# Performance work log

Measured on AMD Instinct MI355X. Metric: run time of the kernel, lower is better.

## Reference

```python
import jax, jax.numpy as jnp
import numpy as np

B = 512          # batch
SD = 1           # series_dim
FEAT = 8         # features_dim
IN = SD + FEAT   # inputs_dim
R = 32           # residual_channels (= skip_channels)
NB, NL = 3, 8
NLAYERS = NB * NL  # 24
L = 256          # cached queue length (>= max dilation 128)
HID = 128        # hidden_size


def setup_inputs() -> dict:
    key = jax.random.key(0)
    ks = jax.random.split(key, 13)
    s = 0.1
    return {
        "x": jax.random.normal(ks[0], (B, SD, 1), jnp.float32),
        "features": jax.random.normal(ks[1], (B, FEAT, 1), jnp.float32),
        "queues": jax.random.normal(ks[2], (NLAYERS, B, R, L), jnp.float32),
        "fc_h_w": jax.random.normal(ks[3], (R, IN), jnp.float32) * s,
        "fc_h_b": jax.random.normal(ks[4], (R,), jnp.float32) * s,
        "fc_c_w": jax.random.normal(ks[5], (R, IN), jnp.float32) * s,
        "fc_c_b": jax.random.normal(ks[6], (R,), jnp.float32) * s,
        "conv_w": jax.random.normal(ks[7], (NLAYERS, 4 * R, R, 2), jnp.float32) * s,
        "conv_b": jax.random.normal(ks[8], (NLAYERS, 4 * R), jnp.float32) * s,
        "fc1_w": jax.random.normal(ks[9], (HID, NLAYERS * R), jnp.float32) * s,
        "fc1_b": jax.random.normal(ks[10], (HID,), jnp.float32) * s,
        "fc2_w": jax.random.normal(ks[11], (SD, HID), jnp.float32) * s,
        "fc2_b": jax.random.normal(ks[12], (SD,), jnp.float32) * s,
    }


def reference(x, features, queues, fc_h_w, fc_h_b, fc_c_w, fc_c_b,
              conv_w, conv_b, fc1_w, fc1_b, fc2_w, fc2_b):
    # inputs: cat over channels at the single decode timestep -> [B, IN]
    inp = jnp.concatenate([x, features], axis=1)[:, :, 0]
    h0 = jnp.tanh(inp @ fc_h_w.T + fc_h_b)   # [B, R]
    c0 = jnp.tanh(inp @ fc_c_w.T + fc_c_b)   # [B, R]

    # dilations 2^0..2^7 repeated for each block; gather the cached sample
    # state[:, :, L-1-(dilation-1)] == state[:, :, L-dilation] for each layer
    dils = jnp.array([2 ** d for _ in range(NB) for d in range(NL)], jnp.int32)
    past = queues[jnp.arange(NLAYERS), :, :, L - dils]   # [NLAYERS, B, R]

    def step(carry, layer):
        h, c = carry
        W, b, p = layer                 # W:[4R,R,2], b:[4R], p:[B,R]
        # kernel-size-2 causal conv on the two timesteps (past, current)
        out = p @ W[:, :, 0].T + h @ W[:, :, 1].T + b    # [B, 4R]
        ig, cf, cg, eg = jnp.split(out, 4, axis=1)
        c = jax.nn.sigmoid(ig) * c + jnp.tanh(cf) * jax.nn.sigmoid(cg)
        h = jax.nn.sigmoid(eg) * jnp.tanh(c)
        return (h, c), h

    (_, _), skips = jax.lax.scan(step, (h0, c0), (conv_w, conv_b, past))
    # skips: [NLAYERS, B, R] -> torch cat(dim=1) order -> [B, NLAYERS*R]
    skips_flat = jnp.transpose(skips, (1, 0, 2)).reshape(B, NLAYERS * R)

    y_hidden = jax.nn.relu(skips_flat @ fc1_w.T + fc1_b)
    h_hat = (y_hidden @ fc2_w.T + fc2_b)[:, :, None]     # [B, SD, 1]

    # update_queues: layer i appends the h ENTERING layer i (h0, then skips[:-1])
    h_seq = jnp.concatenate([h0[None], skips[:-1]], axis=0)  # [NLAYERS, B, R]
    update_queues = jnp.concatenate([queues, h_seq[:, :, :, None]], axis=3)
    return h_hat, update_queues
```

## Files before the change

kernel.cpp:

```cpp
#include <hip/hip_runtime.h>
#include <math.h>

#define B 512
#define FEAT 8
#define IN 9
#define R 32
#define NLAYERS 24
#define L 256
#define HID 128

#define SCAN_BLOCKS 128
#define COPY_BLOCKS 2048
#define ROWS (NLAYERS * B * R)
#define OUTQ_FLOATS (ROWS * 257)
#define NQ (OUTQ_FLOATS / 4)

__device__ __forceinline__ float sigmoidf_(float x) {
    return 1.0f / (1.0f + __expf(-x));
}
__device__ __forceinline__ float tanhf_(float x) {
    float a = __expf(2.0f * fabsf(x));
    float r = 1.0f - 2.0f / (a + 1.0f);
    return copysignf(r, x);
}

__global__ __launch_bounds__(256) void wavedec_scan(
    const float* __restrict__ x, const float* __restrict__ features,
    const float* __restrict__ queues,
    const float* __restrict__ fc_h_w, const float* __restrict__ fc_h_b,
    const float* __restrict__ fc_c_w, const float* __restrict__ fc_c_b,
    const float* __restrict__ conv_w, const float* __restrict__ conv_b,
    const float* __restrict__ fc1_w, const float* __restrict__ fc1_b,
    const float* __restrict__ fc2_w, const float* __restrict__ fc2_b,
    float* __restrict__ out)
{
    const int tid  = threadIdx.x;
    const int lane = tid & 63;
    const int wid  = tid >> 6;
    float* outq = out + B;

    const int b = blockIdx.x * 4 + wid;
    const int r = lane & 31;
    __shared__ __align__(16) float sk[4][NLAYERS * R];

    float inp[IN];
    inp[0] = x[b];
    #pragma unroll
    for (int i = 0; i < FEAT; i++) inp[1 + i] = features[b * FEAT + i];
    float ah = fc_h_b[r], ac = fc_c_b[r];
    #pragma unroll
    for (int i = 0; i < IN; i++) {
        ah += inp[i] * fc_h_w[r * IN + i];
        ac += inp[i] * fc_c_w[r * IN + i];
    }
    float h = tanhf_(ah);
    float c = tanhf_(ac);

    for (int l = 0; l < NLAYERS; l++) {
        const int dil = 1 << (l & 7);
        const int base = (l * B + b) * R;

        if (lane < 32) outq[(long)(base + r) * 257 + 256] = h;

        float p = queues[(long)(base + r) * 256 + (256 - dil)];

        const float* W0 = conv_w + ((long)l * 128 + lane) * 64;
        const float* W1 = W0 + 64 * 64;
        float acc0 = conv_b[l * 128 + lane];
        float acc1 = conv_b[l * 128 + lane + 64];
        #pragma unroll
        for (int rr = 0; rr < 32; rr += 2) {
            float4 wa = *(const float4*)(W0 + rr * 2);
            float4 wb = *(const float4*)(W1 + rr * 2);
            float h0v = __shfl(h, rr),     p0v = __shfl(p, rr);
            float h1v = __shfl(h, rr + 1), p1v = __shfl(p, rr + 1);
            acc0 += p0v * wa.x + h0v * wa.y + p1v * wa.z + h1v * wa.w;
            acc1 += p0v * wb.x + h0v * wb.y + p1v * wb.z + h1v * wb.w;
        }
        float cf = __shfl(acc0, r + 32);
        float eg = __shfl(acc1, r + 32);
        c = sigmoidf_(acc0) * c + tanhf_(cf) * sigmoidf_(acc1);
        h = sigmoidf_(eg) * tanhf_(c);

        if (lane < 32) sk[wid][l * R + r] = h;
    }
    __syncthreads();

    const float* w1a = fc1_w + (long)lane * 768;
    const float* w1b = fc1_w + (long)(lane + 64) * 768;
    const float* skp = sk[wid];
    float ya = fc1_b[lane], yb = fc1_b[lane + 64];
    for (int i = 0; i < 768; i += 4) {
        float4 s  = *(const float4*)(skp + i);
        float4 a4 = *(const float4*)(w1a + i);
        float4 b4 = *(const float4*)(w1b + i);
        ya += s.x * a4.x + s.y * a4.y + s.z * a4.z + s.w * a4.w;
        yb += s.x * b4.x + s.y * b4.y + s.z * b4.z + s.w * b4.w;
    }
    ya = fmaxf(ya, 0.0f);
    yb = fmaxf(yb, 0.0f);
    float v = ya * fc2_w[lane] + yb * fc2_w[lane + 64];
    #pragma unroll
    for (int off = 32; off; off >>= 1) v += __shfl_xor(v, off);
    if (lane == 0) out[b] = v + fc2_b[0];
}

__global__ __launch_bounds__(256) void wavedec_copy(
    const float* __restrict__ queues, float* __restrict__ out)
{
    float* __restrict__ outq = out + B;
    const uint32_t stride = gridDim.x * blockDim.x;
    for (uint32_t q = blockIdx.x * blockDim.x + threadIdx.x; q < (uint32_t)NQ; q += stride) {
        const uint32_t o   = q << 2;
        const uint32_t row = (uint32_t)(((uint64_t)o * 4278255361ull) >> 40);
        const uint32_t col = o - row * 257u;
        float v[4];
        #pragma unroll
        for (int i = 0; i < 4; i++) {
            uint32_t r2 = row, c2 = col + (uint32_t)i;
            if (c2 >= 257u) { r2 += 1u; c2 -= 257u; }
            const float* p = (c2 < 256u)
                ? (queues + (size_t)(r2 << 8) + c2)
                : (outq + (size_t)r2 * 257u + 256u);
            v[i] = *p;
        }
        *(float4*)(outq + (size_t)o) = make_float4(v[0], v[1], v[2], v[3]);
    }
}

extern "C" void kernel_launch(void* const* d_in, const int* in_sizes, int n_in,
                              void* d_out, int out_size, void* d_ws, size_t ws_size,
                              hipStream_t stream)
{
    const float* x        = (const float*)d_in[0];
    const float* features = (const float*)d_in[1];
    const float* queues   = (const float*)d_in[2];
    const float* fc_h_w   = (const float*)d_in[3];
    const float* fc_h_b   = (const float*)d_in[4];
    const float* fc_c_w   = (const float*)d_in[5];
    const float* fc_c_b   = (const float*)d_in[6];
    const float* conv_w   = (const float*)d_in[7];
    const float* conv_b   = (const float*)d_in[8];
    const float* fc1_w    = (const float*)d_in[9];
    const float* fc1_b    = (const float*)d_in[10];
    const float* fc2_w    = (const float*)d_in[11];
    const float* fc2_b    = (const float*)d_in[12];
    float* out = (float*)d_out;

    hipLaunchKernelGGL(wavedec_scan, dim3(SCAN_BLOCKS), dim3(256), 0, stream,
                       x, features, queues, fc_h_w, fc_h_b, fc_c_w, fc_c_b,
                       conv_w, conv_b, fc1_w, fc1_b, fc2_w, fc2_b, out);
    hipLaunchKernelGGL(wavedec_copy, dim3(COPY_BLOCKS), dim3(256), 0, stream,
                       queues, out);
}
```

Baseline: 870.8 us.

## Fuse queue copy into scan kernel with per-wave 4-row group copying

Merges the separate queue-copy kernel into the scan kernel. Extra blocks beyond the scan blocks now copy the cached queues, so the copy overlaps the latency-bound recurrent scan and one launch is saved. The copy is restructured so each wave handles groups of 4 rows (1024 source floats to 1028 destination floats) with mostly aligned float4 stores, instead of a per-element div/mod index computation. The appended h column is written by the scan blocks. The copy blocks must leave those slots untouched, which the copy logic does by skipping column 256, and unaligned source reads may cost some bandwidth.

```diff
diff --git a/kernel.cpp b/kernel.cpp
--- a/kernel.cpp
+++ b/kernel.cpp
@@ -10,10 +10,9 @@
 #define HID 128
 
 #define SCAN_BLOCKS 128
-#define COPY_BLOCKS 2048
+#define COPY_BLOCKS 6144
 #define ROWS (NLAYERS * B * R)
-#define OUTQ_FLOATS (ROWS * 257)
-#define NQ (OUTQ_FLOATS / 4)
+#define GROUPS (ROWS / 4)
 
 __device__ __forceinline__ float sigmoidf_(float x) {
     return 1.0f / (1.0f + __expf(-x));
@@ -24,7 +23,7 @@
     return copysignf(r, x);
 }
 
-__global__ __launch_bounds__(256) void wavedec_scan(
+__global__ __launch_bounds__(256) void wavedec_fused(
     const float* __restrict__ x, const float* __restrict__ features,
     const float* __restrict__ queues,
     const float* __restrict__ fc_h_w, const float* __restrict__ fc_h_b,
@@ -38,6 +37,47 @@
     const int lane = tid & 63;
     const int wid  = tid >> 6;
     float* outq = out + B;
+
+    if (blockIdx.x >= SCAN_BLOCKS) {
+        const int wv = (blockIdx.x - SCAN_BLOCKS) * 4 + wid;
+        #pragma unroll
+        for (int i = 0; i < 4; ++i) {
+            const int g = wv * 4 + i;
+            const float* __restrict__ src = queues + (size_t)g * 1024;
+            float*       __restrict__ dst = outq   + (size_t)g * 1028;
+
+            {
+                const float4 v = *(const float4*)(src + lane * 4);
+                *(float4*)(dst + lane * 4) = v;
+            }
+            #pragma unroll
+            for (int k = 1; k < 4; ++k) {
+                const int f = (k * 64 + lane) * 4;
+                if (lane == 0) {
+                    const int rig = k - 1;
+                    const int c   = f - rig * 257;
+                    #pragma unroll
+                    for (int j = 0; j < 4; ++j) {
+                        const int cj = c + j;
+                        if (cj == 256) continue;
+                        const int s = f + j - rig - (cj > 256 ? 1 : 0);
+                        dst[f + j] = src[s];
+                    }
+                } else {
+                    const int s = f - k;
+                    const float v0 = src[s],     v1 = src[s + 1];
+                    const float v2 = src[s + 2], v3 = src[s + 3];
+                    *(float4*)(dst + f) = make_float4(v0, v1, v2, v3);
+                }
+            }
+            if (lane == 1) {
+                dst[1024] = src[1021];
+                dst[1025] = src[1022];
+                dst[1026] = src[1023];
+            }
+        }
+        return;
+    }
 
     const int b = blockIdx.x * 4 + wid;
     const int r = lane & 31;
@@ -105,29 +145,6 @@
     if (lane == 0) out[b] = v + fc2_b[0];
 }
 
-__global__ __launch_bounds__(256) void wavedec_copy(
-    const float* __restrict__ queues, float* __restrict__ out)
-{
-    float* __restrict__ outq = out + B;
-    const uint32_t stride = gridDim.x * blockDim.x;
-    for (uint32_t q = blockIdx.x * blockDim.x + threadIdx.x; q < (uint32_t)NQ; q += stride) {
-        const uint32_t o   = q << 2;
-        const uint32_t row = (uint32_t)(((uint64_t)o * 4278255361ull) >> 40);
-        const uint32_t col = o - row * 257u;
-        float v[4];
-        #pragma unroll
-        for (int i = 0; i < 4; i++) {
-            uint32_t r2 = row, c2 = col + (uint32_t)i;
-            if (c2 >= 257u) { r2 += 1u; c2 -= 257u; }
-            const float* p = (c2 < 256u)
-                ? (queues + (size_t)(r2 << 8) + c2)
-                : (outq + (size_t)r2 * 257u + 256u);
-            v[i] = *p;
-        }
-        *(float4*)(outq + (size_t)o) = make_float4(v[0], v[1], v[2], v[3]);
-    }
-}
-
 extern "C" void kernel_launch(void* const* d_in, const int* in_sizes, int n_in,
                               void* d_out, int out_size, void* d_ws, size_t ws_size,
                               hipStream_t stream)
@@ -147,9 +164,7 @@
     const float* fc2_b    = (const float*)d_in[12];
     float* out = (float*)d_out;
 
-    hipLaunchKernelGGL(wavedec_scan, dim3(SCAN_BLOCKS), dim3(256), 0, stream,
+    hipLaunchKernelGGL(wavedec_fused, dim3(SCAN_BLOCKS + COPY_BLOCKS), dim3(256), 0, stream,
                        x, features, queues, fc_h_w, fc_h_b, fc_c_w, fc_c_b,
                        conv_w, conv_b, fc1_w, fc1_b, fc2_w, fc2_b, out);
-    hipLaunchKernelGGL(wavedec_copy, dim3(COPY_BLOCKS), dim3(256), 0, stream,
-                       queues, out);
 }
```

Result: faster. 794.5 us (-8.8%).
